# Performance work log

Measured on AMD Instinct MI355X. Metric: run time of the kernel, lower is better.

The kernel has to match this reference:

```python
import jax, jax.numpy as jnp
import numpy as np

B, S, H, NH = 2, 2048, 1024, 16
HD = H // NH  # head_dim = 64


def setup_inputs() -> dict:
    key = jax.random.key(0)
    kx, kl, kq, kk, kv, ko = jax.random.split(key, 6)
    scale = 1.0 / np.sqrt(H)
    return {
        "x": jax.random.normal(kx, (B, S, H), dtype=jnp.float32),
        "seq_lengths": jax.random.randint(kl, (B,), 1, S + 1, dtype=jnp.int32),
        "Wq": jax.random.normal(kq, (H, H), dtype=jnp.float32) * scale,
        "Wk": jax.random.normal(kk, (H, H), dtype=jnp.float32) * scale,
        "Wv": jax.random.normal(kv, (H, H), dtype=jnp.float32) * scale,
        "Wo": jax.random.normal(ko, (H, H), dtype=jnp.float32) * scale,
    }


def reference(x, seq_lengths, Wq, Wk, Wv, Wo):
    b, s, _ = x.shape
    # projections (nn.Linear with no bias: x @ W.T)
    q = (x @ Wq.T).reshape(b, s, NH, HD).transpose(0, 2, 1, 3)  # [b,h,s,d]
    k = (x @ Wk.T).reshape(b, s, NH, HD).transpose(0, 2, 1, 3)
    v = (x @ Wv.T).reshape(b, s, NH, HD).transpose(0, 2, 1, 3)

    scores = jnp.einsum("bhqd,bhkd->bhqk", q, k) / jnp.sqrt(jnp.float32(HD))

    causal = jnp.triu(jnp.ones((s, s), dtype=bool), k=1)[None, None]  # [1,1,s,s]
    padding = (jnp.arange(s)[None, :] >= seq_lengths[:, None])[:, None, None, :]
    mask = causal | padding
    scores = jnp.where(mask, -jnp.inf, scores)

    att = jax.nn.softmax(scores, axis=-1)  # stable: subtract row max once
    out = jnp.einsum("bhqk,bhkd->bhqd", att, v)
    out = out.transpose(0, 2, 1, 3).reshape(b, s, H)
    return out @ Wo.T
```

## Files before the change

kernel.cpp:

```cpp
#include <hip/hip_runtime.h>

typedef unsigned short u16;
typedef short bf16x8 __attribute__((ext_vector_type(8)));
typedef float f32x4 __attribute__((ext_vector_type(4)));

#define DEVINL __device__ __forceinline__

DEVINL u16 f2bf(float f) {
    union { float f; unsigned int u; } x;
    x.f = f;
    unsigned int u = x.u;
    unsigned int r = (u + 0x7fffu + ((u >> 16) & 1u)) >> 16;
    return (u16)r;
}

DEVINL unsigned int cvtpk(float a, float b) {
    unsigned int r;
    asm("v_cvt_pk_bf16_f32 %0, %1, %2" : "=v"(r) : "v"(a), "v"(b));
    return r;
}

DEVINL void async16(const u16* g, u16* l) {
    __builtin_amdgcn_global_load_lds(
        (const __attribute__((address_space(1))) void*)g,
        (__attribute__((address_space(3))) void*)l, 16, 0, 0);
}

DEVINL f32x4 mfma32(bf16x8 a, bf16x8 b, f32x4 c) {
    return __builtin_amdgcn_mfma_f32_16x16x32_bf16(a, b, c, 0, 0, 0);
}

__global__ void pma_cvt_all(const float* __restrict__ x,
                            const float* __restrict__ w0, const float* __restrict__ w1,
                            const float* __restrict__ w2, const float* __restrict__ w3,
                            u16* __restrict__ xb, u16* __restrict__ wdst) {
    const int y = blockIdx.y;
    const int i = blockIdx.x * 256 + threadIdx.x;
    const float4* src;
    ushort4* dst;
    float s = 1.0f;
    if (y < 4) {
        src = (const float4*)x + (size_t)y * 262144;
        dst = (ushort4*)xb + (size_t)y * 262144;
    } else {
        const int wsel = y - 4;
        const float* w = (wsel == 0) ? w0 : (wsel == 1) ? w1 : (wsel == 2) ? w2 : w3;
        src = (const float4*)w;
        dst = (ushort4*)wdst + (size_t)wsel * 262144;
        if (wsel == 0) s = 0.125f;
    }
    float4 v = src[i];
    ushort4 o;
    o.x = f2bf(v.x * s); o.y = f2bf(v.y * s); o.z = f2bf(v.z * s); o.w = f2bf(v.w * s);
    dst[i] = o;
}

__global__ __launch_bounds__(256) void pma_gemm_qkv(
    const u16* __restrict__ A,
    const u16* __restrict__ W0, const u16* __restrict__ W1, const u16* __restrict__ W2,
    u16* __restrict__ O0, u16* __restrict__ O1, u16* __restrict__ Vt,
    const int* __restrict__ seq_lengths)
{
    const int t = threadIdx.x;
    const int lane = t & 63, wave = t >> 6;
    const int m0 = blockIdx.x * 128;
    const int bn = blockIdx.y;
    const int which = bn >> 3;
    const int n0 = (bn & 7) * 128;

    if (which != 0 && (m0 & 2047) >= seq_lengths[m0 >> 11]) return;

    const u16* W = (which == 0) ? W0 : (which == 1) ? W1 : W2;

    __shared__ u16 Alds[128 * 64];
    __shared__ u16 Blds[128 * 64];

    const int wm = wave >> 1, wn = wave & 1;
    const int r16 = lane & 15, g4 = lane >> 4;
    const int r7 = r16 & 7;

    f32x4 acc[4][4];
    const f32x4 z = {0.f, 0.f, 0.f, 0.f};
#pragma unroll
    for (int m = 0; m < 4; ++m)
#pragma unroll
        for (int n = 0; n < 4; ++n) acc[m][n] = z;

    for (int k0 = 0; k0 < 1024; k0 += 64) {
        __syncthreads();
#pragma unroll
        for (int j = 0; j < 4; ++j) {
            int i = j * 256 + t;
            int row = i >> 3, seg = i & 7;
            int sc = ((seg ^ (row & 7)) * 8);
            async16(A + (size_t)(m0 + row) * 1024 + k0 + sc,
                    Alds + (size_t)(j * 256 + wave * 64) * 8);
            async16(W + (size_t)(n0 + row) * 1024 + k0 + sc,
                    Blds + (size_t)(j * 256 + wave * 64) * 8);
        }
        __syncthreads();

#pragma unroll
        for (int half = 0; half < 2; ++half) {
            bf16x8 af[4], bfr[4];
#pragma unroll
            for (int m = 0; m < 4; ++m)
                af[m] = *reinterpret_cast<const bf16x8*>(
                    Alds + (wm * 64 + m * 16 + r16) * 64 + (((half * 4 + g4) ^ r7) * 8));
#pragma unroll
            for (int n = 0; n < 4; ++n)
                bfr[n] = *reinterpret_cast<const bf16x8*>(
                    Blds + (wn * 64 + n * 16 + r16) * 64 + (((half * 4 + g4) ^ r7) * 8));
#pragma unroll
            for (int m = 0; m < 4; ++m)
#pragma unroll
                for (int n = 0; n < 4; ++n)
                    acc[m][n] = mfma32(af[m], bfr[n], acc[m][n]);
        }
    }

    if (which == 2) {
#pragma unroll
        for (int m = 0; m < 4; ++m)
#pragma unroll
            for (int n = 0; n < 4; ++n) {
                int row = m0 + wm * 64 + m * 16 + g4 * 4;
                int col = n0 + wn * 64 + n * 16 + r16;
                ushort4 pk;
                pk.x = f2bf(acc[m][n][0]); pk.y = f2bf(acc[m][n][1]);
                pk.z = f2bf(acc[m][n][2]); pk.w = f2bf(acc[m][n][3]);
                size_t addr = ((size_t)((row >> 11) * 16 + (col >> 6)) * 64 + (col & 63)) * 2048
                              + (row & 2047);
                *reinterpret_cast<ushort4*>(Vt + addr) = pk;
            }
    } else {
        u16* O = (which == 0) ? O0 : O1;
#pragma unroll
        for (int m = 0; m < 4; ++m)
#pragma unroll
            for (int n = 0; n < 4; ++n) {
                int row = m0 + wm * 64 + m * 16 + g4 * 4;
                int col = n0 + wn * 64 + n * 16 + r16;
#pragma unroll
                for (int r = 0; r < 4; ++r)
                    O[(size_t)(row + r) * 1024 + col] = f2bf(acc[m][n][r]);
            }
    }
}

__global__ __launch_bounds__(256) void pma_gemm_wo(
    const u16* __restrict__ A, const u16* __restrict__ W, float* __restrict__ O)
{
    const int t = threadIdx.x;
    const int lane = t & 63, wave = t >> 6;
    const int m0 = blockIdx.x * 64;
    const int n0 = blockIdx.y * 128;

    __shared__ u16 Alds[64 * 32];
    __shared__ u16 Blds[128 * 32];

    const int r16 = lane & 15, g4 = lane >> 4;

    f32x4 acc[4][2];
    const f32x4 z = {0.f, 0.f, 0.f, 0.f};
#pragma unroll
    for (int m = 0; m < 4; ++m) { acc[m][0] = z; acc[m][1] = z; }

    for (int k0 = 0; k0 < 1024; k0 += 32) {
        __syncthreads();
        {
            int row = t >> 2, seg = t & 3;
            async16(A + (size_t)(m0 + row) * 1024 + k0 + seg * 8,
                    Alds + (size_t)(wave * 64) * 8);
        }
#pragma unroll
        for (int j = 0; j < 2; ++j) {
            int i = j * 256 + t;
            int row = i >> 2, seg = i & 3;
            async16(W + (size_t)(n0 + row) * 1024 + k0 + seg * 8,
                    Blds + (size_t)(j * 256 + wave * 64) * 8);
        }
        __syncthreads();

        bf16x8 af[4], bfr[2];
#pragma unroll
        for (int m = 0; m < 4; ++m)
            af[m] = *reinterpret_cast<const bf16x8*>(Alds + (m * 16 + r16) * 32 + g4 * 8);
#pragma unroll
        for (int n = 0; n < 2; ++n)
            bfr[n] = *reinterpret_cast<const bf16x8*>(Blds + (wave * 32 + n * 16 + r16) * 32 + g4 * 8);
#pragma unroll
        for (int m = 0; m < 4; ++m)
#pragma unroll
            for (int n = 0; n < 2; ++n)
                acc[m][n] = mfma32(af[m], bfr[n], acc[m][n]);
    }

#pragma unroll
    for (int m = 0; m < 4; ++m)
#pragma unroll
        for (int n = 0; n < 2; ++n) {
            int row = m0 + m * 16 + g4 * 4;
            int col = n0 + wave * 32 + n * 16 + r16;
#pragma unroll
            for (int r = 0; r < 4; ++r)
                O[(size_t)(row + r) * 1024 + col] = acc[m][n][r];
        }
}

__global__ __launch_bounds__(256, 4) void pma_attn_kernel(
    const u16* __restrict__ Q, const u16* __restrict__ Kp, const u16* __restrict__ Vt,
    const int* __restrict__ seq_lengths, u16* __restrict__ O)
{
    const int bx = blockIdx.x;
    const int qt = 31 - (bx >> 5);
    const int bh = bx & 31;
    const int h  = bh & 15;
    const int b  = bh >> 4;
    const int q0 = qt * 64;
    const int t = threadIdx.x, lane = t & 63, w = t >> 6;
    const int r16 = lane & 15, g4 = lane >> 4;
    const int seqlen = seq_lengths[b];
    const float L2E = 1.4426950408889634f;
    const float NB = 8.0f * L2E;

    __shared__ u16 Klds[2 * 64 * 64];
    __shared__ u16 Vlds[2 * 64 * 64];
    __shared__ u16 Plds[64 * 64];

    const size_t bbase = (size_t)b * 2048 * 1024;
    const size_t hoff = (size_t)h * 64;
    const size_t vrow0 = (size_t)((b * 16 + h) * 64);

    const f32x4 z = {0.f, 0.f, 0.f, 0.f};
    const int krel = t >> 3;
    const int seg  = t & 7;

    const size_t qrowbase = bbase + (size_t)(q0 + w * 16 + r16) * 1024 + hoff;
    const bf16x8 qf0 = *reinterpret_cast<const bf16x8*>(Q + qrowbase + g4 * 8);
    const bf16x8 qf1 = *reinterpret_cast<const bf16x8*>(Q + qrowbase + 32 + g4 * 8);

    bf16x8 vones;
#pragma unroll
    for (int j = 0; j < 8; ++j) vones[j] = (short)0x3F80;

    f32x4 acc[4], accL;
#pragma unroll
    for (int f = 0; f < 4; ++f) acc[f] = z;
    accL = z;

    int kmax = q0 + 63;
    if (seqlen - 1 < kmax) kmax = seqlen - 1;
    const int nt = (kmax >> 6) + 1;

    const u16* kbase = Kp + bbase + hoff + (size_t)krel * 1024 + seg * 8;
    const u16* vbase = Vt + (vrow0 + krel) * 2048 + seg * 8;
    const int stw = krel * 64 + ((seg ^ (krel & 7)) * 8);

    const int r7 = r16 & 7;
    const int kread_lo = r16 * 64 + ((g4 ^ r7) * 8);
    const int kread_hi = r16 * 64 + (((g4 + 4) ^ r7) * 8);
    const int prow = (w * 16 + r16) * 64;

    bf16x8 kreg[2], vreg[2];

#pragma unroll
    for (int j = 0; j < 2; ++j) {
        kreg[j] = *reinterpret_cast<const bf16x8*>(kbase + j * 32 * 1024);
        vreg[j] = *reinterpret_cast<const bf16x8*>(vbase + j * 32 * 2048);
    }
#pragma unroll
    for (int j = 0; j < 2; ++j) {
        *reinterpret_cast<bf16x8*>(Klds + stw + j * 2048) = kreg[j];
        *reinterpret_cast<bf16x8*>(Vlds + stw + j * 2048) = vreg[j];
    }
    __syncthreads();

    const int qhat = q0 + w * 16 + r16;

    for (int tt = 0; tt < nt; ++tt) {
        const int t0 = tt << 6;
        const int dbo = (tt & 1) << 12;
        const int dbn = 4096 - dbo;

        if (tt + 1 < nt) {
            const int t0n = (tt + 1) << 6;
#pragma unroll
            for (int j = 0; j < 2; ++j) {
                kreg[j] = *reinterpret_cast<const bf16x8*>(kbase + (size_t)t0n * 1024 + j * 32 * 1024);
                vreg[j] = *reinterpret_cast<const bf16x8*>(vbase + t0n + j * 32 * 2048);
            }
        }

        f32x4 sraw[4];
        __builtin_amdgcn_s_setprio(1);
#pragma unroll
        for (int kc = 0; kc < 4; ++kc) {
            bf16x8 kf0 = *reinterpret_cast<const bf16x8*>(Klds + dbo + kc * 1024 + kread_lo);
            bf16x8 kf1 = *reinterpret_cast<const bf16x8*>(Klds + dbo + kc * 1024 + kread_hi);
            f32x4 s = z;
            s = mfma32(kf0, qf0, s);
            s = mfma32(kf1, qf1, s);
            sraw[kc] = s;
        }
        __builtin_amdgcn_s_setprio(0);

        float sc[4][4];
        const bool needmask = (t0 == q0) || (t0 + 64 > seqlen);
#pragma unroll
        for (int kc = 0; kc < 4; ++kc)
#pragma unroll
            for (int r = 0; r < 4; ++r)
                sc[kc][r] = exp2f(__builtin_fmaf(sraw[kc][r], L2E, -NB));
        if (needmask) {
#pragma unroll
            for (int kc = 0; kc < 4; ++kc) {
                const int keyb = t0 + kc * 16 + g4 * 4;
#pragma unroll
                for (int r = 0; r < 4; ++r)
                    if ((keyb + r > qhat) || (keyb + r >= seqlen)) sc[kc][r] = 0.f;
            }
        }

#pragma unroll
        for (int kc = 0; kc < 4; ++kc) {
            uint2 pk;
            pk.x = cvtpk(sc[kc][0], sc[kc][1]);
            pk.y = cvtpk(sc[kc][2], sc[kc][3]);
            const int phys16 = (kc * 2 + (g4 >> 1)) ^ r7;
            *reinterpret_cast<uint2*>(Plds + prow + phys16 * 8 + (g4 & 1) * 4) = pk;
        }

        __builtin_amdgcn_s_setprio(1);
#pragma unroll
        for (int kc2 = 0; kc2 < 2; ++kc2) {
            bf16x8 pa = *reinterpret_cast<const bf16x8*>(Plds + prow + (((kc2 * 4 + g4) ^ r7) * 8));
            accL = mfma32(pa, vones, accL);
#pragma unroll
            for (int f = 0; f < 4; ++f) {
                bf16x8 vb = *reinterpret_cast<const bf16x8*>(
                    Vlds + dbo + (f * 16 + r16) * 64 + (((kc2 * 4 + g4) ^ r7) * 8));
                acc[f] = mfma32(pa, vb, acc[f]);
            }
        }
        __builtin_amdgcn_s_setprio(0);

        if (tt + 1 < nt) {
#pragma unroll
            for (int j = 0; j < 2; ++j) {
                *reinterpret_cast<bf16x8*>(Klds + dbn + stw + j * 2048) = kreg[j];
                *reinterpret_cast<bf16x8*>(Vlds + dbn + stw + j * 2048) = vreg[j];
            }
            __syncthreads();
        }
    }

#pragma unroll
    for (int f = 0; f < 4; ++f)
#pragma unroll
        for (int r = 0; r < 4; ++r) {
            int sr = q0 + w * 16 + g4 * 4 + r;
            float o = acc[f][r] / accL[r];
            O[bbase + (size_t)sr * 1024 + hoff + f * 16 + r16] = f2bf(o);
        }
}

extern "C" void kernel_launch(void* const* d_in, const int* in_sizes, int n_in,
                              void* d_out, int out_size, void* d_ws, size_t ws_size,
                              hipStream_t stream) {
    const float* x   = (const float*)d_in[0];
    const int*   sql = (const int*)d_in[1];
    const float* Wq  = (const float*)d_in[2];
    const float* Wk  = (const float*)d_in[3];
    const float* Wv  = (const float*)d_in[4];
    const float* Wo  = (const float*)d_in[5];
    float* out = (float*)d_out;

    const size_t MB = 1024 * 1024;
    char* ws = (char*)d_ws;
    u16* xb   = (u16*)(ws + 0 * MB);
    u16* wqb  = (u16*)(ws + 8 * MB);
    u16* wkb  = (u16*)(ws + 10 * MB);
    u16* wvb  = (u16*)(ws + 12 * MB);
    u16* wob  = (u16*)(ws + 14 * MB);
    u16* Qb   = (u16*)(ws + 16 * MB);
    u16* Kb   = (u16*)(ws + 24 * MB);
    u16* Vtb  = (u16*)(ws + 32 * MB);
    u16* attb = (u16*)(ws + 40 * MB);

    pma_cvt_all<<<dim3(1024, 8), 256, 0, stream>>>(x, Wq, Wk, Wv, Wo, xb, wqb);

    pma_gemm_qkv<<<dim3(32, 24), 256, 0, stream>>>(xb, wqb, wkb, wvb, Qb, Kb, Vtb, sql);

    pma_attn_kernel<<<1024, 256, 0, stream>>>(Qb, Kb, Vtb, sql, attb);

    pma_gemm_wo<<<dim3(64, 8), 256, 0, stream>>>(attb, wob, out);
}
```

Baseline: 113.0 us.

## Double-buffer LDS tiles in QKV and Wo GEMMs with XOR swizzle

Both projection GEMMs now keep two LDS buffers and issue the async global-to-LDS loads for the next K-slice before running MFMAs on the current one, so each iteration has one barrier instead of two. The QKV GEMM's K-step shrinks from 64 to 32 so the doubled buffers fit in the same LDS size. A new XOR swizzle over 4 chunks is applied to the 32-wide rows to reduce LDS bank conflicts, including in the Wo GEMM, which had none before. The risk is that async loads into the next buffer may not be complete at the single barrier unless the compiler inserts the needed vmcnt waits, and there are more loop iterations with less work each.

Result: slower. 121.4 us (+7.4%).

```diff
diff --git a/kernel.cpp b/kernel.cpp
--- a/kernel.cpp
+++ b/kernel.cpp
@@ -72,12 +72,16 @@
 
     const u16* W = (which == 0) ? W0 : (which == 1) ? W1 : W2;
 
-    __shared__ u16 Alds[128 * 64];
-    __shared__ u16 Blds[128 * 64];
+    __shared__ u16 Alds[2 * 128 * 32];
+    __shared__ u16 Blds[2 * 128 * 32];
 
     const int wm = wave >> 1, wn = wave & 1;
     const int r16 = lane & 15, g4 = lane >> 4;
-    const int r7 = r16 & 7;
+    const int rsw = (r16 >> 1) & 3;
+    const int achunk = (g4 ^ rsw) * 8;
+
+    const int srow0 = t >> 2, sseg0 = t & 3;
+    const int scol = (sseg0 ^ ((srow0 >> 1) & 3)) * 8;
 
     f32x4 acc[4][4];
     const f32x4 z = {0.f, 0.f, 0.f, 0.f};
@@ -86,37 +90,46 @@
 #pragma unroll
         for (int n = 0; n < 4; ++n) acc[m][n] = z;
 
-    for (int k0 = 0; k0 < 1024; k0 += 64) {
+#pragma unroll
+    for (int j = 0; j < 2; ++j) {
+        const int row = j * 64 + srow0;
+        async16(A + (size_t)(m0 + row) * 1024 + scol,
+                Alds + (size_t)(j * 256 + wave * 64) * 8);
+        async16(W + (size_t)(n0 + row) * 1024 + scol,
+                Blds + (size_t)(j * 256 + wave * 64) * 8);
+    }
+    __syncthreads();
+
+    for (int tt = 0; tt < 32; ++tt) {
+        const int cur = (tt & 1) << 12;
+        const int nxt = 4096 - cur;
+
+        if (tt + 1 < 32) {
+            const int k0n = (tt + 1) * 32;
+#pragma unroll
+            for (int j = 0; j < 2; ++j) {
+                const int row = j * 64 + srow0;
+                async16(A + (size_t)(m0 + row) * 1024 + k0n + scol,
+                        Alds + nxt + (size_t)(j * 256 + wave * 64) * 8);
+                async16(W + (size_t)(n0 + row) * 1024 + k0n + scol,
+                        Blds + nxt + (size_t)(j * 256 + wave * 64) * 8);
+            }
+        }
+
+        bf16x8 af[4], bfr[4];
+#pragma unroll
+        for (int m = 0; m < 4; ++m)
+            af[m] = *reinterpret_cast<const bf16x8*>(Alds + cur + (wm * 64 + m * 16 + r16) * 32 + achunk);
+#pragma unroll
+        for (int n = 0; n < 4; ++n)
+            bfr[n] = *reinterpret_cast<const bf16x8*>(Blds + cur + (wn * 64 + n * 16 + r16) * 32 + achunk);
+#pragma unroll
+        for (int m = 0; m < 4; ++m)
+#pragma unroll
+            for (int n = 0; n < 4; ++n)
+                acc[m][n] = mfma32(af[m], bfr[n], acc[m][n]);
+
         __syncthreads();
-#pragma unroll
-        for (int j = 0; j < 4; ++j) {
-            int i = j * 256 + t;
-            int row = i >> 3, seg = i & 7;
-            int sc = ((seg ^ (row & 7)) * 8);
-            async16(A + (size_t)(m0 + row) * 1024 + k0 + sc,
-                    Alds + (size_t)(j * 256 + wave * 64) * 8);
-            async16(W + (size_t)(n0 + row) * 1024 + k0 + sc,
-                    Blds + (size_t)(j * 256 + wave * 64) * 8);
-        }
-        __syncthreads();
-
-#pragma unroll
-        for (int half = 0; half < 2; ++half) {
-            bf16x8 af[4], bfr[4];
-#pragma unroll
-            for (int m = 0; m < 4; ++m)
-                af[m] = *reinterpret_cast<const bf16x8*>(
-                    Alds + (wm * 64 + m * 16 + r16) * 64 + (((half * 4 + g4) ^ r7) * 8));
-#pragma unroll
-            for (int n = 0; n < 4; ++n)
-                bfr[n] = *reinterpret_cast<const bf16x8*>(
-                    Blds + (wn * 64 + n * 16 + r16) * 64 + (((half * 4 + g4) ^ r7) * 8));
-#pragma unroll
-            for (int m = 0; m < 4; ++m)
-#pragma unroll
-                for (int n = 0; n < 4; ++n)
-                    acc[m][n] = mfma32(af[m], bfr[n], acc[m][n]);
-        }
     }
 
     if (which == 2) {
@@ -156,44 +169,61 @@
     const int m0 = blockIdx.x * 64;
     const int n0 = blockIdx.y * 128;
 
-    __shared__ u16 Alds[64 * 32];
-    __shared__ u16 Blds[128 * 32];
+    __shared__ u16 Alds[2 * 64 * 32];
+    __shared__ u16 Blds[2 * 128 * 32];
 
     const int r16 = lane & 15, g4 = lane >> 4;
+    const int rsw = (r16 >> 1) & 3;
+    const int achunk = (g4 ^ rsw) * 8;
+
+    const int srow0 = t >> 2, sseg0 = t & 3;
+    const int scol = (sseg0 ^ ((srow0 >> 1) & 3)) * 8;
 
     f32x4 acc[4][2];
     const f32x4 z = {0.f, 0.f, 0.f, 0.f};
 #pragma unroll
     for (int m = 0; m < 4; ++m) { acc[m][0] = z; acc[m][1] = z; }
 
-    for (int k0 = 0; k0 < 1024; k0 += 32) {
-        __syncthreads();
-        {
-            int row = t >> 2, seg = t & 3;
-            async16(A + (size_t)(m0 + row) * 1024 + k0 + seg * 8,
-                    Alds + (size_t)(wave * 64) * 8);
-        }
-#pragma unroll
-        for (int j = 0; j < 2; ++j) {
-            int i = j * 256 + t;
-            int row = i >> 2, seg = i & 3;
-            async16(W + (size_t)(n0 + row) * 1024 + k0 + seg * 8,
-                    Blds + (size_t)(j * 256 + wave * 64) * 8);
-        }
-        __syncthreads();
+    async16(A + (size_t)(m0 + srow0) * 1024 + scol,
+            Alds + (size_t)(wave * 64) * 8);
+#pragma unroll
+    for (int j = 0; j < 2; ++j) {
+        const int row = j * 64 + srow0;
+        async16(W + (size_t)(n0 + row) * 1024 + scol,
+                Blds + (size_t)(j * 256 + wave * 64) * 8);
+    }
+    __syncthreads();
+
+    for (int tt = 0; tt < 32; ++tt) {
+        const int curA = (tt & 1) << 11, nxtA = 2048 - curA;
+        const int curB = (tt & 1) << 12, nxtB = 4096 - curB;
+
+        if (tt + 1 < 32) {
+            const int k0n = (tt + 1) * 32;
+            async16(A + (size_t)(m0 + srow0) * 1024 + k0n + scol,
+                    Alds + nxtA + (size_t)(wave * 64) * 8);
+#pragma unroll
+            for (int j = 0; j < 2; ++j) {
+                const int row = j * 64 + srow0;
+                async16(W + (size_t)(n0 + row) * 1024 + k0n + scol,
+                        Blds + nxtB + (size_t)(j * 256 + wave * 64) * 8);
+            }
+        }
 
         bf16x8 af[4], bfr[2];
 #pragma unroll
         for (int m = 0; m < 4; ++m)
-            af[m] = *reinterpret_cast<const bf16x8*>(Alds + (m * 16 + r16) * 32 + g4 * 8);
+            af[m] = *reinterpret_cast<const bf16x8*>(Alds + curA + (m * 16 + r16) * 32 + achunk);
 #pragma unroll
         for (int n = 0; n < 2; ++n)
-            bfr[n] = *reinterpret_cast<const bf16x8*>(Blds + (wave * 32 + n * 16 + r16) * 32 + g4 * 8);
+            bfr[n] = *reinterpret_cast<const bf16x8*>(Blds + curB + (wave * 32 + n * 16 + r16) * 32 + achunk);
 #pragma unroll
         for (int m = 0; m < 4; ++m)
 #pragma unroll
             for (int n = 0; n < 2; ++n)
                 acc[m][n] = mfma32(af[m], bfr[n], acc[m][n]);
+
+        __syncthreads();
     }
 
 #pragma unroll
```
